# Kernel tuning notes

Hardware: AMD Instinct MI355X
Metric: run time of the kernel (lower is better)

Reference implementation:

```python
import jax, jax.numpy as jnp
import numpy as np

LOC_SIZE, LOC_EMB = 50000, 512
TIM_SIZE, TIM_EMB = 48, 32
UID_SIZE, UID_EMB = 10000, 64
HID = 512
H = HID + TIM_EMB  # 544, odeblock / merge width
N_SEG = 8192
TOTAL = 262144  # sum(history_count)
SEQ = 1024
TLEN = 1024


def setup_inputs() -> dict:
    key = jax.random.key(0)
    ks = jax.random.split(key, 12)
    # history_count: positive ints summing exactly to TOTAL
    rs = np.random.RandomState(0)
    counts = np.full(N_SEG, TOTAL // N_SEG, dtype=np.int32)  # 32 each
    d = rs.randint(0, 16, N_SEG // 2).astype(np.int32)
    counts[: N_SEG // 2] += d
    counts[N_SEG // 2 :] -= d  # min 17, sum preserved
    return {
        "loc": jax.random.randint(ks[0], (SEQ, 1), 0, LOC_SIZE, dtype=jnp.int32),
        "tim": jax.random.randint(ks[1], (SEQ, 1), 0, TIM_SIZE, dtype=jnp.int32),
        "history_loc": jax.random.randint(ks[2], (TOTAL, 1), 0, LOC_SIZE, dtype=jnp.int32),
        "history_tim": jax.random.randint(ks[3], (TOTAL, 1), 0, TIM_SIZE, dtype=jnp.int32),
        "history_count": jnp.asarray(counts),
        "uid": jax.random.randint(ks[4], (1,), 0, UID_SIZE, dtype=jnp.int32),
        "target_len": TLEN,
        "emb_loc_w": jax.random.normal(ks[5], (LOC_SIZE, LOC_EMB), jnp.float32) * 0.02,
        "emb_tim_w": jax.random.normal(ks[6], (TIM_SIZE, TIM_EMB), jnp.float32) * 0.02,
        "emb_uid_w": jax.random.normal(ks[7], (UID_SIZE, UID_EMB), jnp.float32) * 0.02,
        "gru_w": jax.random.normal(ks[8], (3, H, H), jnp.float32) * (1.0 / np.sqrt(H)),
        "gru_b": jnp.zeros((3, H), jnp.float32),
        "fc_final_w": jax.random.normal(ks[9], (H + UID_EMB, LOC_SIZE), jnp.float32) * 0.02,
        "fc_final_b": jnp.zeros((LOC_SIZE,), jnp.float32),
    }


def reference(loc, tim, history_loc, history_tim, history_count, uid, target_len,
              emb_loc_w, emb_tim_w, emb_uid_w, gru_w, gru_b, fc_final_w, fc_final_b):
    # ----- short-term sequence: embed, concat, dot-attention (Attn method='dot') -----
    x = jnp.concatenate([emb_loc_w[loc[:, 0]], emb_tim_w[tim[:, 0]]], axis=-1)  # [S, H]
    x = x[-target_len:]
    attn_w = jax.nn.softmax(x @ x.T, axis=-1)          # vectorized double-loop of Attn
    x_attn = attn_w @ x                                # [T, H]

    # ----- long-term history: variable-length segment mean (the python loop) -----
    loc_eh = emb_loc_w[history_loc[:, 0]]              # [TOTAL, LOC_EMB]
    tim_eh = emb_tim_w[history_tim[:, 0]]              # [TOTAL, TIM_EMB]
    csum = jnp.cumsum(history_count)                   # inclusive offsets
    offsets = csum - history_count                     # segment starts
    seg_ids = jnp.searchsorted(csum, jnp.arange(loc_eh.shape[0]), side="right")
    loc_mean = jax.ops.segment_sum(loc_eh, seg_ids, num_segments=history_count.shape[0])
    loc_mean = loc_mean / history_count[:, None].astype(x.dtype)  # [N_SEG, LOC_EMB]
    tim_first = tim_eh[offsets]                        # first tim of each segment
    history = jnp.concatenate([loc_mean, tim_first], axis=1)      # [N_SEG, H]

    # ----- merge, autonomous GRU-ODE block (single Euler step, dt=1) -----
    h = jnp.concatenate([history, x_attn], axis=0)     # [N_SEG+T, H]
    r = jax.nn.sigmoid(h @ gru_w[0] + gru_b[0])
    z = jax.nn.sigmoid(h @ gru_w[1] + gru_b[1])
    g = jnp.tanh((r * h) @ gru_w[2] + gru_b[2])
    out_state = h + (1.0 - z) * (g - h)                # h + dh (GRU-ODE derivative)

    # ----- output head -----
    out = out_state[-target_len:]
    uid_emb = jnp.broadcast_to(emb_uid_w[uid[0]], (target_len, emb_uid_w.shape[1]))
    y = jnp.concatenate([out, uid_emb], axis=1) @ fc_final_w + fc_final_b  # [T, V]
    return jax.nn.log_softmax(y, axis=-1)
```

## Files before the change

kernel.cpp:

```cpp
#include <hip/hip_runtime.h>
#include <hip/hip_bf16.h>
#include <math.h>

#define SEQ   1024
#define TL    1024
#define DLOC  512
#define DTIM  32
#define DH    544
#define DUID  64
#define DF    608
#define NVOC  50000
#define NT_FINAL 391
#define NPAD  50048

typedef __attribute__((ext_vector_type(8))) short short8;
typedef __attribute__((ext_vector_type(4))) float f32x4;

__device__ __forceinline__ unsigned short f2bf(float f) {
    union { float f; unsigned int u; } x; x.f = f;
    unsigned int u = x.u;
    return (unsigned short)((u + 0x7fffu + ((u >> 16) & 1u)) >> 16);
}

__device__ __forceinline__ void gll16(const unsigned short* g, unsigned short* l) {
    __builtin_amdgcn_global_load_lds(
        (const __attribute__((address_space(1))) void*)g,
        (__attribute__((address_space(3))) void*)l,
        16, 0, 0);
}

template<bool WBF16>
__global__ __launch_bounds__(256) void gemm_bb(
    const unsigned short* __restrict__ A,
    const unsigned short* __restrict__ Bt,
    float* __restrict__ C, unsigned short* __restrict__ Cb,
    int K, int N, int lda, int ldc, int ldcb)
{
    __shared__ __align__(16) unsigned short SMEM[16384];
    const int m0 = blockIdx.y << 7, n0 = blockIdx.x << 7;
    const int tid = threadIdx.x, w = tid >> 6, lane = tid & 63;
    const int wr = (w >> 1) << 6, wc = (w & 1) << 6;
    const int llo = lane & 15, lhi = lane >> 4;

    const int c0 = (w * 2 + 0) * 64 + lane;
    const int c1 = (w * 2 + 1) * 64 + lane;
    const int r0 = c0 >> 2, s0 = (c0 & 3) ^ ((r0 >> 1) & 3);
    const int r1 = c1 >> 2, s1 = (c1 & 3) ^ ((r1 >> 1) & 3);

    f32x4 acc[4][4];
    #pragma unroll
    for (int i = 0; i < 4; ++i)
        #pragma unroll
        for (int j = 0; j < 4; ++j)
            #pragma unroll
            for (int q = 0; q < 4; ++q) acc[i][j][q] = 0.0f;

    auto STAGE = [&](int buf, int kt) {
        const int k0 = kt << 5;
        unsigned short* As = &SMEM[buf * 4096];
        unsigned short* Bs = &SMEM[8192 + buf * 4096];
        gll16(&A [(size_t)(m0 + r0) * lda + k0 + s0 * 8], &As[(w * 2 + 0) * 512]);
        gll16(&A [(size_t)(m0 + r1) * lda + k0 + s1 * 8], &As[(w * 2 + 1) * 512]);
        gll16(&Bt[(size_t)(n0 + r0) * K   + k0 + s0 * 8], &Bs[(w * 2 + 0) * 512]);
        gll16(&Bt[(size_t)(n0 + r1) * K   + k0 + s1 * 8], &Bs[(w * 2 + 1) * 512]);
    };

    const int nk = K >> 5;
    STAGE(0, 0);
    __syncthreads();
    int cur = 0;
    for (int kt = 0; kt < nk; ++kt) {
        if (kt + 1 < nk) STAGE(cur ^ 1, kt + 1);
        const unsigned short* As = &SMEM[cur * 4096];
        const unsigned short* Bs = &SMEM[8192 + cur * 4096];
        short8 af[4], bfv[4];
        #pragma unroll
        for (int fm = 0; fm < 4; ++fm) {
            int row = wr + fm * 16 + llo;
            af[fm] = *reinterpret_cast<const short8*>(&As[row * 32 + (lhi ^ ((row >> 1) & 3)) * 8]);
        }
        #pragma unroll
        for (int fn = 0; fn < 4; ++fn) {
            int row = wc + fn * 16 + llo;
            bfv[fn] = *reinterpret_cast<const short8*>(&Bs[row * 32 + (lhi ^ ((row >> 1) & 3)) * 8]);
        }
        #pragma unroll
        for (int fm = 0; fm < 4; ++fm)
            #pragma unroll
            for (int fn = 0; fn < 4; ++fn)
                acc[fm][fn] = __builtin_amdgcn_mfma_f32_16x16x32_bf16(af[fm], bfv[fn], acc[fm][fn], 0, 0, 0);
        __syncthreads();
        cur ^= 1;
    }

    #pragma unroll
    for (int fm = 0; fm < 4; ++fm)
        #pragma unroll
        for (int fn = 0; fn < 4; ++fn)
            #pragma unroll
            for (int j = 0; j < 4; ++j) {
                int row = m0 + wr + fm * 16 + (lhi << 2) + j;
                int col = n0 + wc + fn * 16 + llo;
                if (col < N) {
                    float v = acc[fm][fn][j];
                    C[(size_t)row * ldc + col] = v;
                    if (WBF16) Cb[(size_t)row * ldcb + col] = f2bf(v);
                }
            }
}

__global__ __launch_bounds__(256) void gemm_final2(
    const unsigned short* __restrict__ Ab,
    const unsigned short* __restrict__ Wt,
    const float* __restrict__ bias,
    float* __restrict__ Y,
    float* __restrict__ Psum)
{
    __shared__ __align__(16) unsigned short SMEM[16384];
    const int bid = blockIdx.x;
    const int wid = (bid & 7) * NT_FINAL + (bid >> 3);
    const int mt = wid & 7, nt = wid >> 3;
    const int m0 = mt << 7, n0 = nt << 7;

    const int tid = threadIdx.x, w = tid >> 6, lane = tid & 63;
    const int wr = (w >> 1) << 6, wc = (w & 1) << 6;
    const int llo = lane & 15, lhi = lane >> 4;

    const int c0 = (w * 2 + 0) * 64 + lane;
    const int c1 = (w * 2 + 1) * 64 + lane;
    const int r0 = c0 >> 2, s0 = (c0 & 3) ^ ((r0 >> 1) & 3);
    const int r1 = c1 >> 2, s1 = (c1 & 3) ^ ((r1 >> 1) & 3);

    f32x4 acc[4][4];
    #pragma unroll
    for (int i = 0; i < 4; ++i)
        #pragma unroll
        for (int j = 0; j < 4; ++j)
            #pragma unroll
            for (int q = 0; q < 4; ++q) acc[i][j][q] = 0.0f;

    auto STAGE = [&](int buf, int kt) {
        const int k0 = kt << 5;
        unsigned short* As = &SMEM[buf * 4096];
        unsigned short* Bs = &SMEM[8192 + buf * 4096];
        gll16(&Ab[(size_t)(m0 + r0) * DF + k0 + s0 * 8], &As[(w * 2 + 0) * 512]);
        gll16(&Ab[(size_t)(m0 + r1) * DF + k0 + s1 * 8], &As[(w * 2 + 1) * 512]);
        gll16(&Wt[(size_t)(n0 + r0) * DF + k0 + s0 * 8], &Bs[(w * 2 + 0) * 512]);
        gll16(&Wt[(size_t)(n0 + r1) * DF + k0 + s1 * 8], &Bs[(w * 2 + 1) * 512]);
    };

    const int nk = DF >> 5;
    STAGE(0, 0);
    __syncthreads();
    int cur = 0;
    for (int kt = 0; kt < nk; ++kt) {
        if (kt + 1 < nk) STAGE(cur ^ 1, kt + 1);
        const unsigned short* As = &SMEM[cur * 4096];
        const unsigned short* Bs = &SMEM[8192 + cur * 4096];
        short8 af[4], bfv[4];
        #pragma unroll
        for (int fm = 0; fm < 4; ++fm) {
            int row = wr + fm * 16 + llo;
            af[fm] = *reinterpret_cast<const short8*>(&As[row * 32 + (lhi ^ ((row >> 1) & 3)) * 8]);
        }
        #pragma unroll
        for (int fn = 0; fn < 4; ++fn) {
            int row = wc + fn * 16 + llo;
            bfv[fn] = *reinterpret_cast<const short8*>(&Bs[row * 32 + (lhi ^ ((row >> 1) & 3)) * 8]);
        }
        #pragma unroll
        for (int fm = 0; fm < 4; ++fm)
            #pragma unroll
            for (int fn = 0; fn < 4; ++fn)
                acc[fm][fn] = __builtin_amdgcn_mfma_f32_16x16x32_bf16(af[fm], bfv[fn], acc[fm][fn], 0, 0, 0);
        __syncthreads();
        cur ^= 1;
    }

    float* red = (float*)SMEM;
    #pragma unroll
    for (int fm = 0; fm < 4; ++fm)
        #pragma unroll
        for (int j = 0; j < 4; ++j) {
            int rowl = wr + fm * 16 + (lhi << 2) + j;
            float s = 0.0f;
            #pragma unroll
            for (int fn = 0; fn < 4; ++fn) {
                int col = n0 + wc + fn * 16 + llo;
                if (col < NVOC) {
                    float v = acc[fm][fn][j] + bias[col];
                    Y[(size_t)(m0 + rowl) * NVOC + col] = v;
                    s += __expf(v);
                }
            }
            red[rowl * 33 + (wc >> 6) * 16 + llo] = s;
        }
    __syncthreads();
    if (tid < 128) {
        float t = 0.0f;
        #pragma unroll
        for (int i = 0; i < 32; ++i) t += red[tid * 33 + i];
        Psum[(size_t)(m0 + tid) * NT_FINAL + nt] = t;
    }
}

__global__ __launch_bounds__(64) void k_combine(
    const float* __restrict__ Psum, float* __restrict__ LSE)
{
    int r = blockIdx.x, lane = threadIdx.x;
    float s = 0.0f;
    for (int i = lane; i < NT_FINAL; i += 64) s += Psum[(size_t)r * NT_FINAL + i];
    #pragma unroll
    for (int off = 32; off >= 1; off >>= 1) s += __shfl_xor(s, off);
    if (lane == 0) LSE[r] = logf(s);
}

__global__ __launch_bounds__(256) void k_cvtW(
    const float* __restrict__ W, unsigned short* __restrict__ Wt)
{
    __shared__ unsigned short T[64][65];
    const int n0 = blockIdx.x * 64, k0 = blockIdx.y * 64;
    const int tid = threadIdx.x;
    #pragma unroll
    for (int i = 0; i < 16; ++i) {
        int idx = i * 256 + tid;
        int kk = idx >> 6, nn = idx & 63;
        int gk = k0 + kk, gn = n0 + nn;
        float v = (gk < DF && gn < NVOC) ? W[(size_t)gk * NVOC + gn] : 0.0f;
        T[nn][kk] = f2bf(v);
    }
    __syncthreads();
    #pragma unroll
    for (int i = 0; i < 16; ++i) {
        int idx = i * 256 + tid;
        int nn = idx >> 6, kk = idx & 63;
        int gk = k0 + kk;
        if (gk < DF) Wt[(size_t)(n0 + nn) * DF + gk] = T[nn][kk];
    }
}

__global__ __launch_bounds__(256) void k_cvtT(
    const float* __restrict__ src, unsigned short* __restrict__ dst,
    int Kdim, int Nvalid, int srcLd)
{
    __shared__ unsigned short T[64][65];
    const int n0 = blockIdx.x * 64, k0 = blockIdx.y * 64;
    const int tid = threadIdx.x;
    #pragma unroll
    for (int i = 0; i < 16; ++i) {
        int idx = i * 256 + tid;
        int kk = idx >> 6, nn = idx & 63;
        int gk = k0 + kk, gn = n0 + nn;
        float v = (gk < Kdim && gn < Nvalid) ? src[(size_t)gk * srcLd + gn] : 0.0f;
        T[nn][kk] = f2bf(v);
    }
    __syncthreads();
    #pragma unroll
    for (int i = 0; i < 16; ++i) {
        int idx = i * 256 + tid;
        int nn = idx >> 6, kk = idx & 63;
        int gk = k0 + kk;
        if (gk < Kdim) dst[(size_t)(n0 + nn) * Kdim + gk] = T[nn][kk];
    }
}

__global__ __launch_bounds__(256) void k_cvtT2(
    const unsigned short* __restrict__ src, unsigned short* __restrict__ dst,
    int Rdim, int Cvalid, int srcLd)
{
    __shared__ unsigned short T[64][65];
    const int c0 = blockIdx.x * 64, r0 = blockIdx.y * 64;
    const int tid = threadIdx.x;
    #pragma unroll
    for (int i = 0; i < 16; ++i) {
        int idx = i * 256 + tid;
        int rr = idx >> 6, cc = idx & 63;
        int gc = c0 + cc;
        T[cc][rr] = (gc < Cvalid) ? src[(size_t)(r0 + rr) * srcLd + gc] : (unsigned short)0;
    }
    __syncthreads();
    #pragma unroll
    for (int i = 0; i < 16; ++i) {
        int idx = i * 256 + tid;
        int cc = idx >> 6, rr = idx & 63;
        dst[(size_t)(c0 + cc) * Rdim + r0 + rr] = T[cc][rr];
    }
}

__global__ __launch_bounds__(256) void k_build_x(
    const int* __restrict__ loc, const int* __restrict__ tim,
    const float* __restrict__ eloc, const float* __restrict__ etim,
    unsigned short* __restrict__ Xb)
{
    int r = blockIdx.x;
    int li = loc[r], ti = tim[r];
    for (int c = threadIdx.x; c < DH; c += 256) {
        float v = (c < DLOC) ? eloc[(size_t)li * DLOC + c]
                             : etim[(size_t)ti * DTIM + (c - DLOC)];
        Xb[(size_t)r * DH + c] = f2bf(v);
    }
}

__global__ __launch_bounds__(256) void k_softmax(
    const float* __restrict__ S, unsigned short* __restrict__ Pb)
{
    int r = blockIdx.x;
    const float* row = S + (size_t)r * SEQ;
    int tid = threadIdx.x;
    float v[4];
    float m = -INFINITY;
    #pragma unroll
    for (int i = 0; i < 4; ++i) { v[i] = row[tid + i * 256]; m = fmaxf(m, v[i]); }
    #pragma unroll
    for (int off = 32; off >= 1; off >>= 1) m = fmaxf(m, __shfl_xor(m, off));
    __shared__ float red[8];
    int w = tid >> 6;
    if ((tid & 63) == 0) red[w] = m;
    __syncthreads();
    m = fmaxf(fmaxf(red[0], red[1]), fmaxf(red[2], red[3]));
    float s = 0.0f;
    #pragma unroll
    for (int i = 0; i < 4; ++i) { v[i] = __expf(v[i] - m); s += v[i]; }
    #pragma unroll
    for (int off = 32; off >= 1; off >>= 1) s += __shfl_xor(s, off);
    __syncthreads();
    if ((tid & 63) == 0) red[4 + w] = s;
    __syncthreads();
    s = red[4] + red[5] + red[6] + red[7];
    float inv = 1.0f / s;
    #pragma unroll
    for (int i = 0; i < 4; ++i)
        Pb[(size_t)r * SEQ + tid + i * 256] = f2bf(v[i] * inv);
}

__global__ __launch_bounds__(256) void k_rh(
    const float* __restrict__ A01, const float* __restrict__ Hf,
    const float* __restrict__ b0, unsigned short* __restrict__ RHb)
{
    int idx = blockIdx.x * 256 + threadIdx.x;
    if (idx >= TL * DH) return;
    int r = idx / DH, c = idx - r * DH;
    float a = A01[(size_t)r * 1088 + c];
    float rg = 1.0f / (1.0f + __expf(-(a + b0[c])));
    RHb[idx] = f2bf(rg * Hf[idx]);
}

__global__ __launch_bounds__(256) void k_out_b(
    const float* __restrict__ A01, const float* __restrict__ GP,
    const float* __restrict__ Hf, const float* __restrict__ b1,
    const float* __restrict__ b2, unsigned short* __restrict__ Ab)
{
    int idx = blockIdx.x * 256 + threadIdx.x;
    if (idx >= TL * DH) return;
    int r = idx / DH, c = idx - r * DH;
    float z = 1.0f / (1.0f + __expf(-(A01[(size_t)r * 1088 + DH + c] + b1[c])));
    float g = tanhf(GP[idx] + b2[c]);
    float h = Hf[idx];
    Ab[(size_t)r * DF + c] = f2bf(h + (1.0f - z) * (g - h));
}

__global__ __launch_bounds__(256) void k_uid_b(
    const int* __restrict__ uid, const float* __restrict__ euid,
    unsigned short* __restrict__ Ab)
{
    int idx = blockIdx.x * 256 + threadIdx.x;
    if (idx >= TL * DUID) return;
    int r = idx >> 6, c = idx & 63;
    Ab[(size_t)r * DF + DH + c] = f2bf(euid[(size_t)uid[0] * DUID + c]);
}

__global__ __launch_bounds__(256) void k_sub(
    float* __restrict__ Y, const float* __restrict__ lse)
{
    int r = blockIdx.y;
    int c4 = blockIdx.x * 256 + threadIdx.x;
    if (c4 >= NVOC / 4) return;
    float l = lse[r];
    float4* p = reinterpret_cast<float4*>(Y + (size_t)r * NVOC);
    float4 v = p[c4];
    v.x -= l; v.y -= l; v.z -= l; v.w -= l;
    p[c4] = v;
}

extern "C" void kernel_launch(void* const* d_in, const int* in_sizes, int n_in,
                              void* d_out, int out_size, void* d_ws, size_t ws_size,
                              hipStream_t stream)
{
    const int*   loc  = (const int*)d_in[0];
    const int*   tim  = (const int*)d_in[1];
    const int*   uid  = (const int*)d_in[5];
    const float* eloc = (const float*)d_in[7];
    const float* etim = (const float*)d_in[8];
    const float* euid = (const float*)d_in[9];
    const float* gru_w = (const float*)d_in[10];
    const float* gru_b = (const float*)d_in[11];
    const float* fcw  = (const float*)d_in[12];
    const float* fcb  = (const float*)d_in[13];
    float* Y = (float*)d_out;

    const float* b0 = gru_b;
    const float* b1 = gru_b + DH;
    const float* b2 = gru_b + 2 * DH;

    float* S    = (float*)d_ws;
    float* Hf   = S    + (size_t)SEQ * SEQ;
    float* A01  = Hf   + (size_t)TL * DH;
    float* GP   = A01  + (size_t)TL * 1088;
    float* Psum = GP   + (size_t)TL * DH;
    float* LSE  = Psum + (size_t)TL * NT_FINAL;
    unsigned short* Xb   = (unsigned short*)(LSE + 1024);
    unsigned short* Xt   = Xb   + (size_t)TL * DH;
    unsigned short* Pb   = Xt   + (size_t)640 * 1024;
    unsigned short* Hb   = Pb   + (size_t)SEQ * SEQ;
    unsigned short* RHb  = Hb   + (size_t)TL * DH;
    unsigned short* Ab   = RHb  + (size_t)TL * DH;
    unsigned short* W01t = Ab   + (size_t)TL * DF;
    unsigned short* W2t  = W01t + (size_t)1184 * DH;
    unsigned short* Wt   = W2t  + (size_t)640 * DH;

    k_cvtW<<<dim3(NPAD / 64, 10), 256, 0, stream>>>(fcw, Wt);
    k_cvtT<<<dim3(9, 9),  256, 0, stream>>>(gru_w,                     W01t,                   DH, DH, DH);
    k_cvtT<<<dim3(10, 9), 256, 0, stream>>>(gru_w + (size_t)DH * DH,   W01t + (size_t)DH * DH, DH, DH, DH);
    k_cvtT<<<dim3(10, 9), 256, 0, stream>>>(gru_w + 2*(size_t)DH * DH, W2t,                    DH, DH, DH);

    k_build_x<<<TL, 256, 0, stream>>>(loc, tim, eloc, etim, Xb);
    k_cvtT2<<<dim3(10, 16), 256, 0, stream>>>(Xb, Xt, TL, DH, DH);

    gemm_bb<false><<<dim3(8, 8), 256, 0, stream>>>(Xb, Xb, S, nullptr, DH, SEQ, DH, SEQ, 0);
    k_softmax<<<SEQ, 256, 0, stream>>>(S, Pb);
    gemm_bb<true><<<dim3(5, 8), 256, 0, stream>>>(Pb, Xt, Hf, Hb, SEQ, DH, SEQ, DH, DH);

    gemm_bb<false><<<dim3(9, 8), 256, 0, stream>>>(Hb, W01t, A01, nullptr, DH, 1088, DH, 1088, 0);
    k_rh<<<(TL * DH + 255) / 256, 256, 0, stream>>>(A01, Hf, b0, RHb);
    gemm_bb<false><<<dim3(5, 8), 256, 0, stream>>>(RHb, W2t, GP, nullptr, DH, DH, DH, DH, 0);
    k_out_b<<<(TL * DH + 255) / 256, 256, 0, stream>>>(A01, GP, Hf, b1, b2, Ab);
    k_uid_b<<<(TL * DUID + 255) / 256, 256, 0, stream>>>(uid, euid, Ab);

    gemm_final2<<<8 * NT_FINAL, 256, 0, stream>>>(Ab, Wt, fcb, Y, Psum);
    k_combine<<<TL, 64, 0, stream>>>(Psum, LSE);
    k_sub<<<dim3((NVOC / 4 + 255) / 256, TL), 256, 0, stream>>>(Y, LSE);
}
```

Measured before the change: 666.0 us.

## Deepen GEMM pipeline, fuse GRU epilogues, recompute final GEMM for log-softmax

The GEMMs move from a 2-stage double buffer to a 4-buffer, 3-deep prefetch pipeline using explicit vmcnt waits and MFMA priority raising. The GRU elementwise kernels (reset gate, output update) are folded into the GEMM epilogues. The final projection now runs twice, once for row exp-sums and once writing bias-minus-LSE outputs, replacing the separate read-modify-write subtraction pass over the 1024x50000 output. The fc weight conversion kernel is also vectorised. Recomputing the large GEMM trades extra MFMA work and weight reads for avoiding one full re-read and re-write of the fp32 output.

```diff
diff --git a/kernel.cpp b/kernel.cpp
--- a/kernel.cpp
+++ b/kernel.cpp
@@ -15,6 +15,11 @@
 
 typedef __attribute__((ext_vector_type(8))) short short8;
 typedef __attribute__((ext_vector_type(4))) float f32x4;
+typedef __attribute__((ext_vector_type(4))) unsigned short u16x4;
+
+#define WAITV8 asm volatile("s_waitcnt vmcnt(8)" ::: "memory")
+#define WAITV4 asm volatile("s_waitcnt vmcnt(4)" ::: "memory")
+#define WAITV0 asm volatile("s_waitcnt vmcnt(0)" ::: "memory")
 
 __device__ __forceinline__ unsigned short f2bf(float f) {
     union { float f; unsigned int u; } x; x.f = f;
@@ -29,23 +34,27 @@
         16, 0, 0);
 }
 
-template<bool WBF16>
-__global__ __launch_bounds__(256) void gemm_bb(
+enum { EPI_S = 0, EPI_PV = 1, EPI_G1 = 2, EPI_G2 = 3 };
+
+template<int EPI>
+__global__ __launch_bounds__(256) void gemm_p(
     const unsigned short* __restrict__ A,
     const unsigned short* __restrict__ Bt,
-    float* __restrict__ C, unsigned short* __restrict__ Cb,
-    int K, int N, int lda, int ldc, int ldcb)
-{
-    __shared__ __align__(16) unsigned short SMEM[16384];
+    int K, int N, int lda, int ldo,
+    float* __restrict__ o1, unsigned short* __restrict__ o2,
+    const float* __restrict__ p1, const float* __restrict__ p2,
+    const float* __restrict__ p3, const float* __restrict__ p4)
+{
+    __shared__ __align__(16) unsigned short SMEM[32768];
     const int m0 = blockIdx.y << 7, n0 = blockIdx.x << 7;
     const int tid = threadIdx.x, w = tid >> 6, lane = tid & 63;
     const int wr = (w >> 1) << 6, wc = (w & 1) << 6;
     const int llo = lane & 15, lhi = lane >> 4;
 
-    const int c0 = (w * 2 + 0) * 64 + lane;
-    const int c1 = (w * 2 + 1) * 64 + lane;
-    const int r0 = c0 >> 2, s0 = (c0 & 3) ^ ((r0 >> 1) & 3);
-    const int r1 = c1 >> 2, s1 = (c1 & 3) ^ ((r1 >> 1) & 3);
+    const int ch0 = (w * 2 + 0) * 64 + lane;
+    const int ch1 = (w * 2 + 1) * 64 + lane;
+    const int r0 = ch0 >> 2, s0 = (ch0 & 3) ^ ((r0 >> 1) & 3);
+    const int r1 = ch1 >> 2, s1 = (ch1 & 3) ^ ((r1 >> 1) & 3);
 
     f32x4 acc[4][4];
     #pragma unroll
@@ -58,7 +67,7 @@
     auto STAGE = [&](int buf, int kt) {
         const int k0 = kt << 5;
         unsigned short* As = &SMEM[buf * 4096];
-        unsigned short* Bs = &SMEM[8192 + buf * 4096];
+        unsigned short* Bs = &SMEM[16384 + buf * 4096];
         gll16(&A [(size_t)(m0 + r0) * lda + k0 + s0 * 8], &As[(w * 2 + 0) * 512]);
         gll16(&A [(size_t)(m0 + r1) * lda + k0 + s1 * 8], &As[(w * 2 + 1) * 512]);
         gll16(&Bt[(size_t)(n0 + r0) * K   + k0 + s0 * 8], &Bs[(w * 2 + 0) * 512]);
@@ -66,13 +75,13 @@
     };
 
     const int nk = K >> 5;
-    STAGE(0, 0);
-    __syncthreads();
-    int cur = 0;
-    for (int kt = 0; kt < nk; ++kt) {
-        if (kt + 1 < nk) STAGE(cur ^ 1, kt + 1);
-        const unsigned short* As = &SMEM[cur * 4096];
-        const unsigned short* Bs = &SMEM[8192 + cur * 4096];
+    STAGE(0, 0); STAGE(1, 1); STAGE(2, 2);
+    WAITV8;
+    __builtin_amdgcn_s_barrier();
+
+    for (int t = 0; t < nk; ++t) {
+        const unsigned short* As = &SMEM[(t & 3) * 4096];
+        const unsigned short* Bs = &SMEM[16384 + (t & 3) * 4096];
         short8 af[4], bfv[4];
         #pragma unroll
         for (int fm = 0; fm < 4; ++fm) {
@@ -84,13 +93,20 @@
             int row = wc + fn * 16 + llo;
             bfv[fn] = *reinterpret_cast<const short8*>(&Bs[row * 32 + (lhi ^ ((row >> 1) & 3)) * 8]);
         }
+        if (t + 3 < nk) STAGE((t + 3) & 3, t + 3);
+        __builtin_amdgcn_s_setprio(1);
         #pragma unroll
         for (int fm = 0; fm < 4; ++fm)
             #pragma unroll
             for (int fn = 0; fn < 4; ++fn)
                 acc[fm][fn] = __builtin_amdgcn_mfma_f32_16x16x32_bf16(af[fm], bfv[fn], acc[fm][fn], 0, 0, 0);
-        __syncthreads();
-        cur ^= 1;
+        __builtin_amdgcn_s_setprio(0);
+        if (t + 1 < nk) {
+            if (t + 3 < nk)      WAITV8;
+            else if (t + 2 < nk) WAITV4;
+            else                 WAITV0;
+            __builtin_amdgcn_s_barrier();
+        }
     }
 
     #pragma unroll
@@ -101,22 +117,42 @@
             for (int j = 0; j < 4; ++j) {
                 int row = m0 + wr + fm * 16 + (lhi << 2) + j;
                 int col = n0 + wc + fn * 16 + llo;
-                if (col < N) {
-                    float v = acc[fm][fn][j];
-                    C[(size_t)row * ldc + col] = v;
-                    if (WBF16) Cb[(size_t)row * ldcb + col] = f2bf(v);
+                float v = acc[fm][fn][j];
+                if (EPI == EPI_S) {
+                    if (col < N) o1[(size_t)row * ldo + col] = v;
+                } else if (EPI == EPI_PV) {
+                    if (col < N) {
+                        o1[(size_t)row * ldo + col] = v;
+                        o2[(size_t)row * ldo + col] = f2bf(v);
+                    }
+                } else if (EPI == EPI_G1) {
+                    if (col < DH) {
+                        float rg = 1.0f / (1.0f + __expf(-(v + p1[col])));
+                        o2[(size_t)row * ldo + col] = f2bf(rg * p2[(size_t)row * DH + col]);
+                    } else if (col < N) {
+                        o1[(size_t)row * ldo + (col - DH)] = v;
+                    }
+                } else {
+                    if (col < N) {
+                        float z = 1.0f / (1.0f + __expf(-(p3[(size_t)row * DH + col] + p1[col])));
+                        float g = tanhf(v + p2[col]);
+                        float h = p4[(size_t)row * DH + col];
+                        o2[(size_t)row * ldo + col] = f2bf(h + (1.0f - z) * (g - h));
+                    }
                 }
             }
 }
 
-__global__ __launch_bounds__(256) void gemm_final2(
+template<int PASS>
+__global__ __launch_bounds__(256) void gemm_fin(
     const unsigned short* __restrict__ Ab,
     const unsigned short* __restrict__ Wt,
     const float* __restrict__ bias,
     float* __restrict__ Y,
-    float* __restrict__ Psum)
-{
-    __shared__ __align__(16) unsigned short SMEM[16384];
+    float* __restrict__ Psum,
+    const float* __restrict__ LSE)
+{
+    __shared__ __align__(16) unsigned short SMEM[32768];
     const int bid = blockIdx.x;
     const int wid = (bid & 7) * NT_FINAL + (bid >> 3);
     const int mt = wid & 7, nt = wid >> 3;
@@ -126,10 +162,10 @@
     const int wr = (w >> 1) << 6, wc = (w & 1) << 6;
     const int llo = lane & 15, lhi = lane >> 4;
 
-    const int c0 = (w * 2 + 0) * 64 + lane;
-    const int c1 = (w * 2 + 1) * 64 + lane;
-    const int r0 = c0 >> 2, s0 = (c0 & 3) ^ ((r0 >> 1) & 3);
-    const int r1 = c1 >> 2, s1 = (c1 & 3) ^ ((r1 >> 1) & 3);
+    const int ch0 = (w * 2 + 0) * 64 + lane;
+    const int ch1 = (w * 2 + 1) * 64 + lane;
+    const int r0 = ch0 >> 2, s0 = (ch0 & 3) ^ ((r0 >> 1) & 3);
+    const int r1 = ch1 >> 2, s1 = (ch1 & 3) ^ ((r1 >> 1) & 3);
 
     f32x4 acc[4][4];
     #pragma unroll
@@ -142,7 +178,7 @@
     auto STAGE = [&](int buf, int kt) {
         const int k0 = kt << 5;
         unsigned short* As = &SMEM[buf * 4096];
-        unsigned short* Bs = &SMEM[8192 + buf * 4096];
+        unsigned short* Bs = &SMEM[16384 + buf * 4096];
         gll16(&Ab[(size_t)(m0 + r0) * DF + k0 + s0 * 8], &As[(w * 2 + 0) * 512]);
         gll16(&Ab[(size_t)(m0 + r1) * DF + k0 + s1 * 8], &As[(w * 2 + 1) * 512]);
         gll16(&Wt[(size_t)(n0 + r0) * DF + k0 + s0 * 8], &Bs[(w * 2 + 0) * 512]);
@@ -150,13 +186,13 @@
     };
 
     const int nk = DF >> 5;
-    STAGE(0, 0);
-    __syncthreads();
-    int cur = 0;
-    for (int kt = 0; kt < nk; ++kt) {
-        if (kt + 1 < nk) STAGE(cur ^ 1, kt + 1);
-        const unsigned short* As = &SMEM[cur * 4096];
-        const unsigned short* Bs = &SMEM[8192 + cur * 4096];
+    STAGE(0, 0); STAGE(1, 1); STAGE(2, 2);
+    WAITV8;
+    __builtin_amdgcn_s_barrier();
+
+    for (int t = 0; t < nk; ++t) {
+        const unsigned short* As = &SMEM[(t & 3) * 4096];
+        const unsigned short* Bs = &SMEM[16384 + (t & 3) * 4096];
         short8 af[4], bfv[4];
         #pragma unroll
         for (int fm = 0; fm < 4; ++fm) {
@@ -168,39 +204,59 @@
             int row = wc + fn * 16 + llo;
             bfv[fn] = *reinterpret_cast<const short8*>(&Bs[row * 32 + (lhi ^ ((row >> 1) & 3)) * 8]);
         }
+        if (t + 3 < nk) STAGE((t + 3) & 3, t + 3);
+        __builtin_amdgcn_s_setprio(1);
         #pragma unroll
         for (int fm = 0; fm < 4; ++fm)
             #pragma unroll
             for (int fn = 0; fn < 4; ++fn)
                 acc[fm][fn] = __builtin_amdgcn_mfma_f32_16x16x32_bf16(af[fm], bfv[fn], acc[fm][fn], 0, 0, 0);
+        __builtin_amdgcn_s_setprio(0);
+        if (t + 1 < nk) {
+            if (t + 3 < nk)      WAITV8;
+            else if (t + 2 < nk) WAITV4;
+            else                 WAITV0;
+            __builtin_amdgcn_s_barrier();
+        }
+    }
+
+    if (PASS == 1) {
         __syncthreads();
-        cur ^= 1;
-    }
-
-    float* red = (float*)SMEM;
-    #pragma unroll
-    for (int fm = 0; fm < 4; ++fm)
-        #pragma unroll
-        for (int j = 0; j < 4; ++j) {
-            int rowl = wr + fm * 16 + (lhi << 2) + j;
-            float s = 0.0f;
-            #pragma unroll
-            for (int fn = 0; fn < 4; ++fn) {
-                int col = n0 + wc + fn * 16 + llo;
-                if (col < NVOC) {
-                    float v = acc[fm][fn][j] + bias[col];
-                    Y[(size_t)(m0 + rowl) * NVOC + col] = v;
-                    s += __expf(v);
+        float* red = (float*)SMEM;
+        #pragma unroll
+        for (int fm = 0; fm < 4; ++fm)
+            #pragma unroll
+            for (int j = 0; j < 4; ++j) {
+                int rowl = wr + fm * 16 + (lhi << 2) + j;
+                float s = 0.0f;
+                #pragma unroll
+                for (int fn = 0; fn < 4; ++fn) {
+                    int col = n0 + wc + fn * 16 + llo;
+                    if (col < NVOC) s += __expf(acc[fm][fn][j] + bias[col]);
+                }
+                red[rowl * 33 + (wc >> 6) * 16 + llo] = s;
+            }
+        __syncthreads();
+        if (tid < 128) {
+            float t2 = 0.0f;
+            #pragma unroll
+            for (int i = 0; i < 32; ++i) t2 += red[tid * 33 + i];
+            Psum[(size_t)(m0 + tid) * NT_FINAL + nt] = t2;
+        }
+    } else {
+        #pragma unroll
+        for (int fm = 0; fm < 4; ++fm)
+            #pragma unroll
+            for (int j = 0; j < 4; ++j) {
+                int rowl = wr + fm * 16 + (lhi << 2) + j;
+                float l = LSE[m0 + rowl];
+                #pragma unroll
+                for (int fn = 0; fn < 4; ++fn) {
+                    int col = n0 + wc + fn * 16 + llo;
+                    if (col < NVOC)
+                        Y[(size_t)(m0 + rowl) * NVOC + col] = acc[fm][fn][j] + bias[col] - l;
                 }
             }
-            red[rowl * 33 + (wc >> 6) * 16 + llo] = s;
-        }
-    __syncthreads();
-    if (tid < 128) {
-        float t = 0.0f;
-        #pragma unroll
-        for (int i = 0; i < 32; ++i) t += red[tid * 33 + i];
-        Psum[(size_t)(m0 + tid) * NT_FINAL + nt] = t;
     }
 }
 
@@ -222,20 +278,28 @@
     const int n0 = blockIdx.x * 64, k0 = blockIdx.y * 64;
     const int tid = threadIdx.x;
     #pragma unroll
-    for (int i = 0; i < 16; ++i) {
-        int idx = i * 256 + tid;
-        int kk = idx >> 6, nn = idx & 63;
-        int gk = k0 + kk, gn = n0 + nn;
-        float v = (gk < DF && gn < NVOC) ? W[(size_t)gk * NVOC + gn] : 0.0f;
-        T[nn][kk] = f2bf(v);
-    }
-    __syncthreads();
-    #pragma unroll
-    for (int i = 0; i < 16; ++i) {
-        int idx = i * 256 + tid;
-        int nn = idx >> 6, kk = idx & 63;
-        int gk = k0 + kk;
-        if (gk < DF) Wt[(size_t)(n0 + nn) * DF + gk] = T[nn][kk];
+    for (int i = 0; i < 4; ++i) {
+        int idx = i * 256 + tid;
+        int kk = idx >> 4;
+        int nq = (idx & 15) << 2;
+        int gk = k0 + kk, gn = n0 + nq;
+        float4 v;
+        if (gk < DF && gn < NVOC) v = *reinterpret_cast<const float4*>(&W[(size_t)gk * NVOC + gn]);
+        else { v.x = v.y = v.z = v.w = 0.0f; }
+        T[nq + 0][kk] = f2bf(v.x); T[nq + 1][kk] = f2bf(v.y);
+        T[nq + 2][kk] = f2bf(v.z); T[nq + 3][kk] = f2bf(v.w);
+    }
+    __syncthreads();
+    #pragma unroll
+    for (int i = 0; i < 4; ++i) {
+        int idx = i * 256 + tid;
+        int nn = idx >> 4;
+        int kq = (idx & 15) << 2;
+        int gk = k0 + kq;
+        if (gk < DF) {
+            u16x4 o; o[0] = T[nn][kq]; o[1] = T[nn][kq + 1]; o[2] = T[nn][kq + 2]; o[3] = T[nn][kq + 3];
+            *reinterpret_cast<u16x4*>(&Wt[(size_t)(n0 + nn) * DF + gk]) = o;
+        }
     }
 }
 
@@ -333,32 +397,6 @@
         Pb[(size_t)r * SEQ + tid + i * 256] = f2bf(v[i] * inv);
 }
 
-__global__ __launch_bounds__(256) void k_rh(
-    const float* __restrict__ A01, const float* __restrict__ Hf,
-    const float* __restrict__ b0, unsigned short* __restrict__ RHb)
-{
-    int idx = blockIdx.x * 256 + threadIdx.x;
-    if (idx >= TL * DH) return;
-    int r = idx / DH, c = idx - r * DH;
-    float a = A01[(size_t)r * 1088 + c];
-    float rg = 1.0f / (1.0f + __expf(-(a + b0[c])));
-    RHb[idx] = f2bf(rg * Hf[idx]);
-}
-
-__global__ __launch_bounds__(256) void k_out_b(
-    const float* __restrict__ A01, const float* __restrict__ GP,
-    const float* __restrict__ Hf, const float* __restrict__ b1,
-    const float* __restrict__ b2, unsigned short* __restrict__ Ab)
-{
-    int idx = blockIdx.x * 256 + threadIdx.x;
-    if (idx >= TL * DH) return;
-    int r = idx / DH, c = idx - r * DH;
-    float z = 1.0f / (1.0f + __expf(-(A01[(size_t)r * 1088 + DH + c] + b1[c])));
-    float g = tanhf(GP[idx] + b2[c]);
-    float h = Hf[idx];
-    Ab[(size_t)r * DF + c] = f2bf(h + (1.0f - z) * (g - h));
-}
-
 __global__ __launch_bounds__(256) void k_uid_b(
     const int* __restrict__ uid, const float* __restrict__ euid,
     unsigned short* __restrict__ Ab)
@@ -367,19 +405,6 @@
     if (idx >= TL * DUID) return;
     int r = idx >> 6, c = idx & 63;
     Ab[(size_t)r * DF + DH + c] = f2bf(euid[(size_t)uid[0] * DUID + c]);
-}
-
-__global__ __launch_bounds__(256) void k_sub(
-    float* __restrict__ Y, const float* __restrict__ lse)
-{
-    int r = blockIdx.y;
-    int c4 = blockIdx.x * 256 + threadIdx.x;
-    if (c4 >= NVOC / 4) return;
-    float l = lse[r];
-    float4* p = reinterpret_cast<float4*>(Y + (size_t)r * NVOC);
-    float4 v = p[c4];
-    v.x -= l; v.y -= l; v.z -= l; v.w -= l;
-    p[c4] = v;
 }
 
 extern "C" void kernel_launch(void* const* d_in, const int* in_sizes, int n_in,
@@ -404,9 +429,8 @@
 
     float* S    = (float*)d_ws;
     float* Hf   = S    + (size_t)SEQ * SEQ;
-    float* A01  = Hf   + (size_t)TL * DH;
-    float* GP   = A01  + (size_t)TL * 1088;
-    float* Psum = GP   + (size_t)TL * DH;
+    float* A01z = Hf   + (size_t)TL * DH;
+    float* Psum = A01z + (size_t)TL * DH;
     float* LSE  = Psum + (size_t)TL * NT_FINAL;
     unsigned short* Xb   = (unsigned short*)(LSE + 1024);
     unsigned short* Xt   = Xb   + (size_t)TL * DH;
@@ -426,17 +450,19 @@
     k_build_x<<<TL, 256, 0, stream>>>(loc, tim, eloc, etim, Xb);
     k_cvtT2<<<dim3(10, 16), 256, 0, stream>>>(Xb, Xt, TL, DH, DH);
 
-    gemm_bb<false><<<dim3(8, 8), 256, 0, stream>>>(Xb, Xb, S, nullptr, DH, SEQ, DH, SEQ, 0);
+    gemm_p<EPI_S><<<dim3(8, 8), 256, 0, stream>>>(
+        Xb, Xb, DH, SEQ, DH, SEQ, S, nullptr, nullptr, nullptr, nullptr, nullptr);
     k_softmax<<<SEQ, 256, 0, stream>>>(S, Pb);
-    gemm_bb<true><<<dim3(5, 8), 256, 0, stream>>>(Pb, Xt, Hf, Hb, SEQ, DH, SEQ, DH, DH);
-
-    gemm_bb<false><<<dim3(9, 8), 256, 0, stream>>>(Hb, W01t, A01, nullptr, DH, 1088, DH, 1088, 0);
-    k_rh<<<(TL * DH + 255) / 256, 256, 0, stream>>>(A01, Hf, b0, RHb);
-    gemm_bb<false><<<dim3(5, 8), 256, 0, stream>>>(RHb, W2t, GP, nullptr, DH, DH, DH, DH, 0);
-    k_out_b<<<(TL * DH + 255) / 256, 256, 0, stream>>>(A01, GP, Hf, b1, b2, Ab);
+    gemm_p<EPI_PV><<<dim3(5, 8), 256, 0, stream>>>(
+        Pb, Xt, SEQ, DH, SEQ, DH, Hf, Hb, nullptr, nullptr, nullptr, nullptr);
+
+    gemm_p<EPI_G1><<<dim3(9, 8), 256, 0, stream>>>(
+        Hb, W01t, DH, 1088, DH, DH, A01z, RHb, b0, Hf, nullptr, nullptr);
+    gemm_p<EPI_G2><<<dim3(5, 8), 256, 0, stream>>>(
+        RHb, W2t, DH, DH, DH, DF, nullptr, Ab, b1, b2, A01z, Hf);
     k_uid_b<<<(TL * DUID + 255) / 256, 256, 0, stream>>>(uid, euid, Ab);
 
-    gemm_final2<<<8 * NT_FINAL, 256, 0, stream>>>(Ab, Wt, fcb, Y, Psum);
+    gemm_fin<1><<<8 * NT_FINAL, 256, 0, stream>>>(Ab, Wt, fcb, Y, Psum, nullptr);
     k_combine<<<TL, 64, 0, stream>>>(Psum, LSE);
-    k_sub<<<dim3((NVOC / 4 + 255) / 256, TL), 256, 0, stream>>>(Y, LSE);
-}
+    gemm_fin<2><<<8 * NT_FINAL, 256, 0, stream>>>(Ab, Wt, fcb, Y, Psum, LSE);
+}
```

Result: slower. 720.0 us (+8.1%).
